# Optimization experiments

Measured on AMD Instinct MI355X. Metric: run time of the kernel, lower is better.

The kernel has to match this reference:

```python
import jax, jax.numpy as jnp
import numpy as np

HIDDEN = 2048
N_HEADS = 32
N_KV_HEADS = 8
HEAD_DIM = HIDDEN // N_HEADS  # 64
KV_GROUPS = N_HEADS // N_KV_HEADS  # 4
ROPE_THETA = 10000.0
BSZ, SEQ = 2, 2048


def setup_inputs() -> dict:
    key = jax.random.key(0)
    ks = jax.random.split(key, 5)
    s = 0.02
    hidden_states = jax.random.normal(ks[0], (BSZ, SEQ, HIDDEN), jnp.float32)
    position_ids = jnp.broadcast_to(jnp.arange(SEQ, dtype=jnp.int32), (BSZ, SEQ))
    Wq = jax.random.normal(ks[1], (HIDDEN, HIDDEN), jnp.float32) * s
    Wk = jax.random.normal(ks[2], (N_KV_HEADS * HEAD_DIM, HIDDEN), jnp.float32) * s
    Wv = jax.random.normal(ks[3], (N_KV_HEADS * HEAD_DIM, HIDDEN), jnp.float32) * s
    Wo = jax.random.normal(ks[4], (HIDDEN, HIDDEN), jnp.float32) * s
    return {"hidden_states": hidden_states, "position_ids": position_ids,
            "Wq": Wq, "Wk": Wk, "Wv": Wv, "Wo": Wo}


def _rope_cos_sin(position_ids):
    # Llama rotary embedding: inv_freq over even dims, emb = [freqs, freqs]
    inv_freq = 1.0 / (ROPE_THETA ** (jnp.arange(0, HEAD_DIM, 2, dtype=jnp.float32) / HEAD_DIM))  # [Hd/2]
    freqs = position_ids.astype(jnp.float32)[..., None] * inv_freq  # [B, S, Hd/2]
    emb = jnp.concatenate([freqs, freqs], axis=-1)  # [B, S, Hd]
    return jnp.cos(emb), jnp.sin(emb)


def _rotate_half(x):
    x1, x2 = jnp.split(x, 2, axis=-1)
    return jnp.concatenate([-x2, x1], axis=-1)


def reference(hidden_states, position_ids, Wq, Wk, Wv, Wo):
    bsz, seq_len, _ = hidden_states.shape
    # projections (nn.Linear: y = x @ W.T)
    q = (hidden_states @ Wq.T).reshape(bsz, seq_len, N_HEADS, HEAD_DIM).transpose(0, 2, 1, 3)
    k = (hidden_states @ Wk.T).reshape(bsz, seq_len, N_KV_HEADS, HEAD_DIM).transpose(0, 2, 1, 3)
    v = (hidden_states @ Wv.T).reshape(bsz, seq_len, N_KV_HEADS, HEAD_DIM).transpose(0, 2, 1, 3)
    cos, sin = _rope_cos_sin(position_ids)  # [B, S, Hd]
    cos = cos[:, None, :, :]
    sin = sin[:, None, :, :]
    q = q * cos + _rotate_half(q) * sin
    k = k * cos + _rotate_half(k) * sin
    # GQA expand kv heads to full head count
    k = jnp.repeat(k, KV_GROUPS, axis=1)  # [B, H, S, Hd]
    v = jnp.repeat(v, KV_GROUPS, axis=1)
    # naive full-softmax attention (no causal mask, matching the source)
    scores = jnp.einsum('bhqd,bhkd->bhqk', q, k) / jnp.sqrt(jnp.float32(HEAD_DIM))
    attn_w = jax.nn.softmax(scores, axis=-1)
    attn_o = jnp.einsum('bhqk,bhkd->bhqd', attn_w, v)
    attn_o = attn_o.transpose(0, 2, 1, 3).reshape(bsz, seq_len, HIDDEN)
    return attn_o @ Wo.T
```

## Files before the change

### kernel.cpp

```cpp
#include <hip/hip_runtime.h>
#include <hip/hip_bf16.h>
#include <stdint.h>

#define HID 2048
#define NH 32
#define NKV 8
#define HD 64
#define BSZ 2
#define SEQ 2048
#define NROWS (BSZ*SEQ)
#define KVCOLS (NKV*HD)
#define QKVN 3072

typedef __attribute__((ext_vector_type(8))) short bf16x8;
typedef __attribute__((ext_vector_type(4))) float f32x4;
typedef __attribute__((ext_vector_type(16))) float f32x16;
typedef __attribute__((ext_vector_type(2))) unsigned int u32x2;

__device__ __forceinline__ unsigned short f2bf(float f) {
  union { float f; uint32_t u; } v; v.f = f;
  uint32_t r = v.u + 0x7FFFu + ((v.u >> 16) & 1u);
  return (unsigned short)(r >> 16);
}

__device__ __forceinline__ unsigned pack_bf16(float a, float b) {
  union { __hip_bfloat162 h; unsigned u; } cv;
  cv.h = __float22bfloat162_rn(make_float2(a, b));
  return cv.u;
}

__device__ __forceinline__ float sum16(const f32x16& s) {
  float a0 = s[0] + s[1], a1 = s[2] + s[3], a2 = s[4] + s[5], a3 = s[6] + s[7];
  float a4 = s[8] + s[9], a5 = s[10] + s[11], a6 = s[12] + s[13], a7 = s[14] + s[15];
  float b0 = a0 + a1, b1 = a2 + a3, b2 = a4 + a5, b3 = a6 + a7;
  return (b0 + b1) + (b2 + b3);
}

#define MKPB(S, B0) ({ \
  unsigned A_ = pack_bf16((S)[B0], (S)[(B0)+1]); \
  unsigned C_ = pack_bf16((S)[(B0)+2], (S)[(B0)+3]); \
  unsigned B_ = pack_bf16((S)[(B0)+4], (S)[(B0)+5]); \
  unsigned D_ = pack_bf16((S)[(B0)+6], (S)[(B0)+7]); \
  u32x2 r0_ = __builtin_amdgcn_permlane32_swap(A_, B_, false, false); \
  u32x2 r1_ = __builtin_amdgcn_permlane32_swap(C_, D_, false, false); \
  union { uint4 u; bf16x8 v; } cv_; \
  cv_.u.x = r0_.x; cv_.u.y = r1_.x; cv_.u.z = r0_.y; cv_.u.w = r1_.y; \
  cv_.v; })

__global__ __launch_bounds__(256) void cvt_kernel(const float* __restrict__ in,
                                                  unsigned short* __restrict__ out, int n) {
  int idx = (blockIdx.x * 256 + threadIdx.x) * 4;
  int stride = gridDim.x * 256 * 4;
  for (int i = idx; i < n; i += stride) {
    float4 v = *(const float4*)(in + i);
    ushort4 o;
    o.x = f2bf(v.x); o.y = f2bf(v.y); o.z = f2bf(v.z); o.w = f2bf(v.w);
    *(ushort4*)(out + i) = o;
  }
}

#define BM 128
#define BN 128
#define BK 32

__global__ __launch_bounds__(256) void gemm_btn(
    const unsigned short* __restrict__ A,
    const unsigned short* __restrict__ B,
    float* __restrict__ C,
    int M, int N, int K)
{
  __shared__ unsigned short As[2][BM * BK];
  __shared__ unsigned short Bs[2][BN * BK];
  const int t = threadIdx.x;
  const int w = t >> 6, l = t & 63;
  const int wr = w >> 1, wc = w & 1;

  const int nwg = gridDim.x * gridDim.y;
  const int lin = blockIdx.y * gridDim.x + blockIdx.x;
  const int swz = (lin & 7) * (nwg >> 3) + (lin >> 3);
  const int bx = swz % gridDim.x, by = swz / gridDim.x;

  const int row0 = by * BM, col0 = bx * BN;
  const int lr = l & 15, lk = (l >> 4) * 8;

  f32x4 acc[4][4];
  for (int i = 0; i < 4; ++i)
    for (int j = 0; j < 4; ++j)
      acc[i][j] = (f32x4){0.f, 0.f, 0.f, 0.f};

  auto stage = [&](int bi, int k0) {
    #pragma unroll
    for (int i = 0; i < 2; ++i) {
      int ebase = i * 2048 + w * 512;
      int e = ebase + l * 8;
      const unsigned short* srcA = A + (size_t)(row0 + (e >> 5)) * K + k0 + (e & 31);
      const unsigned short* srcB = B + (size_t)(col0 + (e >> 5)) * K + k0 + (e & 31);
      __builtin_amdgcn_global_load_lds((const __attribute__((address_space(1))) void*)srcA,
          (__attribute__((address_space(3))) void*)&As[bi][ebase], 16, 0, 0);
      __builtin_amdgcn_global_load_lds((const __attribute__((address_space(1))) void*)srcB,
          (__attribute__((address_space(3))) void*)&Bs[bi][ebase], 16, 0, 0);
    }
  };

  stage(0, 0);
  __syncthreads();
  int bi = 0;
  for (int k0 = 0; k0 < K; k0 += BK) {
    if (k0 + BK < K) stage(bi ^ 1, k0 + BK);
    bf16x8 a[4], b[4];
    #pragma unroll
    for (int mi = 0; mi < 4; ++mi)
      a[mi] = *(const bf16x8*)&As[bi][(wr * 64 + mi * 16 + lr) * BK + lk];
    #pragma unroll
    for (int ni = 0; ni < 4; ++ni)
      b[ni] = *(const bf16x8*)&Bs[bi][(wc * 64 + ni * 16 + lr) * BK + lk];
    #pragma unroll
    for (int mi = 0; mi < 4; ++mi)
      #pragma unroll
      for (int ni = 0; ni < 4; ++ni)
        acc[mi][ni] = __builtin_amdgcn_mfma_f32_16x16x32_bf16(a[mi], b[ni], acc[mi][ni], 0, 0, 0);
    __syncthreads();
    bi ^= 1;
  }

  const int crow = (l >> 4) * 4, ccol = l & 15;
  #pragma unroll
  for (int mi = 0; mi < 4; ++mi)
    #pragma unroll
    for (int ni = 0; ni < 4; ++ni) {
      float* cp = C + (size_t)(row0 + wr * 64 + mi * 16 + crow) * N + col0 + wc * 64 + ni * 16 + ccol;
      #pragma unroll
      for (int r = 0; r < 4; ++r)
        cp[(size_t)r * N] = acc[mi][ni][r];
    }
}

__global__ __launch_bounds__(256) void rope_k_kernel(const float* __restrict__ QKVf,
                                                     const int* __restrict__ pos_ids,
                                                     unsigned short* __restrict__ Kb) {
  int row = blockIdx.x;
  int t = threadIdx.x;
  int kh = t >> 5, j = t & 31;
  int b = row >> 11, s = row & 2047;
  float pos = (float)pos_ids[row];
  float invf = exp2f((float)j * -0.41524101186092029f);
  float sn, c;
  __sincosf(pos * invf, &sn, &c);
  const float* kr = QKVf + (size_t)row * QKVN + HID + kh * 64;
  float k1 = kr[j], k2 = kr[j + 32];
  float o1 = k1 * c - k2 * sn;
  float o2 = k2 * c + k1 * sn;
  unsigned short* outp = Kb + ((size_t)(b * NKV + kh) * SEQ + s) * HD;
  outp[j] = f2bf(o1);
  outp[j + 32] = f2bf(o2);
}

__global__ __launch_bounds__(256) void vt_kernel(const float* __restrict__ QKVf,
                                                 unsigned short* __restrict__ Vt) {
  int bid = blockIdx.x;
  int stile = bid & 31;
  int kh = (bid >> 5) & 7;
  int b = bid >> 8;
  int s0 = stile * 64;
  __shared__ unsigned short Ts[64][65];
  int t = threadIdx.x;
  {
    int r = t >> 2;
    int dq = (t & 3) * 16;
    const float* src = QKVf + (size_t)(b * SEQ + s0 + r) * QKVN + (HID + KVCOLS) + kh * 64 + dq;
    #pragma unroll
    for (int i = 0; i < 4; ++i) {
      float4 v = *(const float4*)(src + i * 4);
      Ts[r][dq + i * 4 + 0] = f2bf(v.x);
      Ts[r][dq + i * 4 + 1] = f2bf(v.y);
      Ts[r][dq + i * 4 + 2] = f2bf(v.z);
      Ts[r][dq + i * 4 + 3] = f2bf(v.w);
    }
  }
  __syncthreads();
  {
    int d = t >> 2;
    int cb = (t & 3) * 16;
    unsigned short* dst = Vt + ((size_t)(b * NKV + kh) * 64 + d) * SEQ + s0 + cb;
    #pragma unroll
    for (int i = 0; i < 4; ++i) {
      ushort4 o;
      o.x = Ts[cb + i * 4 + 0][d];
      o.y = Ts[cb + i * 4 + 1][d];
      o.z = Ts[cb + i * 4 + 2][d];
      o.w = Ts[cb + i * 4 + 3][d];
      *(ushort4*)(dst + i * 4) = o;
    }
  }
}

__global__ __launch_bounds__(512, 4) void attn_kernel(
    const float* __restrict__ QKVf,
    const int* __restrict__ pos_ids,
    const unsigned short* __restrict__ Kb,
    const unsigned short* __restrict__ Vt,
    unsigned short* __restrict__ AO)
{
  __shared__ unsigned short Ks[2][64 * 64];
  __shared__ unsigned short Vs[2][64 * 64];

  const int lin = blockIdx.x;
  const int bid = (lin & 7) * 64 + (lin >> 3);
  const int qtile = bid & 7;
  const int h = (bid >> 3) & 31;
  const int b = bid >> 8;
  const int kh = h >> 2;
  const int t = threadIdx.x, w = t >> 6, l = t & 63;
  const int lq = l & 31, hi = l >> 5;
  const int sw = (lq & 7) << 4;
  const int qrow = qtile * 256 + w * 32 + lq;

  bf16x8 qf[4];
  {
    const float SCL = 0.18033688011112042f;
    const float* Qsrc = QKVf + (size_t)(b * SEQ + qrow) * QKVN + h * 64;
    float pos = (float)pos_ids[b * SEQ + qrow];
    #pragma unroll
    for (int dk = 0; dk < 2; ++dk) {
      float4 a0 = *(const float4*)(Qsrc + dk * 16 + hi * 8);
      float4 a1 = *(const float4*)(Qsrc + dk * 16 + hi * 8 + 4);
      float4 b0 = *(const float4*)(Qsrc + 32 + dk * 16 + hi * 8);
      float4 b1 = *(const float4*)(Qsrc + 32 + dk * 16 + hi * 8 + 4);
      float x1[8] = {a0.x, a0.y, a0.z, a0.w, a1.x, a1.y, a1.z, a1.w};
      float x2[8] = {b0.x, b0.y, b0.z, b0.w, b1.x, b1.y, b1.z, b1.w};
      union { bf16x8 v; unsigned short us[8]; } lov, hiv;
      #pragma unroll
      for (int jj = 0; jj < 8; ++jj) {
        float jidx = (float)(dk * 16 + hi * 8 + jj);
        float sn, cs;
        __sincosf(pos * exp2f(jidx * -0.41524101186092029f), &sn, &cs);
        lov.us[jj] = f2bf((x1[jj] * cs - x2[jj] * sn) * SCL);
        hiv.us[jj] = f2bf((x2[jj] * cs + x1[jj] * sn) * SCL);
      }
      qf[dk] = lov.v;
      qf[dk + 2] = hiv.v;
    }
  }

  const unsigned short* Kt  = Kb + (size_t)(b * NKV + kh) * SEQ * HD;
  const unsigned short* Vth = Vt + (size_t)(b * NKV + kh) * HD * SEQ;

  const int dest = t * 16;
  const int srow = dest >> 7;
  const int scol = dest & 127;
  const int wdest = dest ^ ((srow & 7) << 4);
  const char* KsrcBase = (const char*)Kt + dest;
  const char* VsrcBase = (const char*)(Vth + (size_t)srow * SEQ) + scol;

  uint4 kreg, vreg;
  auto issue = [&](int kv0) {
    kreg = *(const uint4*)(KsrcBase + (size_t)kv0 * 128);
    vreg = *(const uint4*)(VsrcBase + kv0 * 2);
  };
  auto lwrite = [&](int si) {
    *(uint4*)((char*)Ks[si] + wdest) = kreg;
    *(uint4*)((char*)Vs[si] + wdest) = vreg;
  };

  const f32x16 Z = {0,0,0,0,0,0,0,0,0,0,0,0,0,0,0,0};
  float lsum = 0.f;
  f32x16 o0 = Z, o1 = Z;

  issue(0);
  lwrite(0);
  __syncthreads();

  int bi = 0;
  for (int it = 0; it < SEQ / 64; ++it) {
    const bool more = (it + 1 < SEQ / 64);
    if (more) issue((it + 1) * 64);

    const char* Kp = (const char*)Ks[bi];
    const char* Vp = (const char*)Vs[bi];

    f32x16 s0, s1;
    __builtin_amdgcn_s_setprio(1);
    {
      bf16x8 kf0 = *(const bf16x8*)(Kp + lq * 128 + ((hi * 16) ^ sw));
      bf16x8 kf1 = *(const bf16x8*)(Kp + 4096 + lq * 128 + ((hi * 16) ^ sw));
      s0 = __builtin_amdgcn_mfma_f32_32x32x16_bf16(kf0, qf[0], Z, 0, 0, 0);
      s1 = __builtin_amdgcn_mfma_f32_32x32x16_bf16(kf1, qf[0], Z, 0, 0, 0);
    }
    #pragma unroll
    for (int dk = 1; dk < 4; ++dk) {
      const int cb = dk * 32 + hi * 16;
      bf16x8 kf0 = *(const bf16x8*)(Kp + lq * 128 + (cb ^ sw));
      bf16x8 kf1 = *(const bf16x8*)(Kp + 4096 + lq * 128 + (cb ^ sw));
      s0 = __builtin_amdgcn_mfma_f32_32x32x16_bf16(kf0, qf[dk], s0, 0, 0, 0);
      s1 = __builtin_amdgcn_mfma_f32_32x32x16_bf16(kf1, qf[dk], s1, 0, 0, 0);
    }
    __builtin_amdgcn_s_setprio(0);

    #pragma unroll
    for (int r = 0; r < 16; ++r) { s0[r] = exp2f(s0[r]); s1[r] = exp2f(s1[r]); }
    float rs = sum16(s0) + sum16(s1);
    rs += __shfl_xor(rs, 32);
    lsum += rs;

    bf16x8 pb0 = MKPB(s0, 0), pb1 = MKPB(s0, 8), pb2 = MKPB(s1, 0), pb3 = MKPB(s1, 8);

    __builtin_amdgcn_s_setprio(1);
    #pragma unroll
    for (int ks = 0; ks < 4; ++ks) {
      const int cb = ks * 32 + hi * 16;
      bf16x8 vf0 = *(const bf16x8*)(Vp + lq * 128 + (cb ^ sw));
      bf16x8 vf1 = *(const bf16x8*)(Vp + 4096 + lq * 128 + (cb ^ sw));
      bf16x8 pa = (ks == 0) ? pb0 : (ks == 1) ? pb1 : (ks == 2) ? pb2 : pb3;
      o0 = __builtin_amdgcn_mfma_f32_32x32x16_bf16(vf0, pa, o0, 0, 0, 0);
      o1 = __builtin_amdgcn_mfma_f32_32x32x16_bf16(vf1, pa, o1, 0, 0, 0);
    }
    __builtin_amdgcn_s_setprio(0);

    if (more) lwrite(bi ^ 1);
    __syncthreads();
    bi ^= 1;
  }

  const float inv = 1.0f / lsum;
  unsigned short* op = AO + ((size_t)(b * SEQ) + qrow) * HID + h * 64;
  #pragma unroll
  for (int r = 0; r < 16; r += 2) {
    const int d = (r & 3) + 8 * (r >> 2) + 4 * hi;
    *(unsigned*)(op + d)      = pack_bf16(o0[r] * inv, o0[r + 1] * inv);
    *(unsigned*)(op + 32 + d) = pack_bf16(o1[r] * inv, o1[r + 1] * inv);
  }
}

extern "C" void kernel_launch(void* const* d_in, const int* in_sizes, int n_in,
                              void* d_out, int out_size, void* d_ws, size_t ws_size,
                              hipStream_t stream) {
  const float* hs  = (const float*)d_in[0];
  const int*   pos = (const int*)d_in[1];
  const float* Wq  = (const float*)d_in[2];
  const float* Wk  = (const float*)d_in[3];
  const float* Wv  = (const float*)d_in[4];
  const float* Wo  = (const float*)d_in[5];
  float* out = (float*)d_out;

  char* ws = (char*)d_ws;
  size_t off = 0;
  auto carve = [&](size_t bytes) { void* p = ws + off; off += (bytes + 255) & ~(size_t)255; return p; };

  unsigned short* Xb    = (unsigned short*)carve((size_t)NROWS * HID * 2);
  unsigned short* Wqkvb = (unsigned short*)carve((size_t)QKVN * HID * 2);
  unsigned short* Wob   = (unsigned short*)carve((size_t)HID * HID * 2);
  float*          QKVf  = (float*)carve((size_t)NROWS * QKVN * 4);
  unsigned short* Kbh   = (unsigned short*)carve((size_t)NROWS * KVCOLS * 2);
  unsigned short* Vtb   = (unsigned short*)carve((size_t)NROWS * KVCOLS * 2);
  unsigned short* AO    = (unsigned short*)carve((size_t)NROWS * HID * 2);

  cvt_kernel<<<1024, 256, 0, stream>>>(hs, Xb, NROWS * HID);
  cvt_kernel<<<512, 256, 0, stream>>>(Wq, Wqkvb, HID * HID);
  cvt_kernel<<<256, 256, 0, stream>>>(Wk, Wqkvb + (size_t)HID * HID, KVCOLS * HID);
  cvt_kernel<<<256, 256, 0, stream>>>(Wv, Wqkvb + (size_t)(HID + KVCOLS) * HID, KVCOLS * HID);
  cvt_kernel<<<512, 256, 0, stream>>>(Wo, Wob, HID * HID);

  gemm_btn<<<dim3(QKVN / BN, NROWS / BM), 256, 0, stream>>>(Xb, Wqkvb, QKVf, NROWS, QKVN, HID);

  rope_k_kernel<<<NROWS, 256, 0, stream>>>(QKVf, pos, Kbh);
  vt_kernel<<<BSZ * NKV * (SEQ / 64), 256, 0, stream>>>(QKVf, Vtb);

  attn_kernel<<<BSZ * NH * (SEQ / 256), 512, 0, stream>>>(QKVf, pos, Kbh, Vtb, AO);

  gemm_btn<<<dim3(HID / BN, NROWS / BM), 256, 0, stream>>>(AO, Wob, out, NROWS, HID, HID);
}
```

Measured before the change: 256.1 us.

## Fuse RoPE, Q scaling and V transpose into the QKV GEMM epilogue

```diff
diff --git a/kernel.cpp b/kernel.cpp
--- a/kernel.cpp
+++ b/kernel.cpp
@@ -46,6 +46,9 @@
   union { uint4 u; bf16x8 v; } cv_; \
   cv_.u.x = r0_.x; cv_.u.y = r1_.x; cv_.u.z = r0_.y; cv_.u.w = r1_.y; \
   cv_.v; })
+
+#define ROPE_C (-0.41524101186092029f)
+#define QSCL 0.18033688011112042f
 
 __global__ __launch_bounds__(256) void cvt_kernel(const float* __restrict__ in,
                                                   unsigned short* __restrict__ out, int n) {
@@ -135,68 +138,122 @@
     }
 }
 
-__global__ __launch_bounds__(256) void rope_k_kernel(const float* __restrict__ QKVf,
-                                                     const int* __restrict__ pos_ids,
-                                                     unsigned short* __restrict__ Kb) {
-  int row = blockIdx.x;
-  int t = threadIdx.x;
-  int kh = t >> 5, j = t & 31;
-  int b = row >> 11, s = row & 2047;
-  float pos = (float)pos_ids[row];
-  float invf = exp2f((float)j * -0.41524101186092029f);
-  float sn, c;
-  __sincosf(pos * invf, &sn, &c);
-  const float* kr = QKVf + (size_t)row * QKVN + HID + kh * 64;
-  float k1 = kr[j], k2 = kr[j + 32];
-  float o1 = k1 * c - k2 * sn;
-  float o2 = k2 * c + k1 * sn;
-  unsigned short* outp = Kb + ((size_t)(b * NKV + kh) * SEQ + s) * HD;
-  outp[j] = f2bf(o1);
-  outp[j + 32] = f2bf(o2);
-}
-
-__global__ __launch_bounds__(256) void vt_kernel(const float* __restrict__ QKVf,
-                                                 unsigned short* __restrict__ Vt) {
-  int bid = blockIdx.x;
-  int stile = bid & 31;
-  int kh = (bid >> 5) & 7;
-  int b = bid >> 8;
-  int s0 = stile * 64;
-  __shared__ unsigned short Ts[64][65];
-  int t = threadIdx.x;
-  {
-    int r = t >> 2;
-    int dq = (t & 3) * 16;
-    const float* src = QKVf + (size_t)(b * SEQ + s0 + r) * QKVN + (HID + KVCOLS) + kh * 64 + dq;
-    #pragma unroll
-    for (int i = 0; i < 4; ++i) {
-      float4 v = *(const float4*)(src + i * 4);
-      Ts[r][dq + i * 4 + 0] = f2bf(v.x);
-      Ts[r][dq + i * 4 + 1] = f2bf(v.y);
-      Ts[r][dq + i * 4 + 2] = f2bf(v.z);
-      Ts[r][dq + i * 4 + 3] = f2bf(v.w);
-    }
-  }
+__global__ __launch_bounds__(256) void gemm_qkv(
+    const unsigned short* __restrict__ A,
+    const unsigned short* __restrict__ B,
+    const int* __restrict__ pos_ids,
+    unsigned short* __restrict__ Qb,
+    unsigned short* __restrict__ Kb,
+    unsigned short* __restrict__ Vt)
+{
+  __shared__ unsigned short As[2][BM * BK];
+  __shared__ unsigned short Bs[2][BN * BK];
+  const int t = threadIdx.x;
+  const int w = t >> 6, l = t & 63;
+  const int wr = w >> 1, wc = w & 1;
+
+  const int nwg = gridDim.x * gridDim.y;
+  const int lin = blockIdx.y * gridDim.x + blockIdx.x;
+  const int swz = (lin & 7) * (nwg >> 3) + (lin >> 3);
+  const int bx = swz % gridDim.x, by = swz / gridDim.x;
+
+  const int row0 = by * BM, col0 = bx * BN;
+  const int lr = l & 15, lk = (l >> 4) * 8;
+
+  f32x4 acc[4][4];
+  for (int i = 0; i < 4; ++i)
+    for (int j = 0; j < 4; ++j)
+      acc[i][j] = (f32x4){0.f, 0.f, 0.f, 0.f};
+
+  auto stage = [&](int bi, int k0) {
+    #pragma unroll
+    for (int i = 0; i < 2; ++i) {
+      int ebase = i * 2048 + w * 512;
+      int e = ebase + l * 8;
+      const unsigned short* srcA = A + (size_t)(row0 + (e >> 5)) * HID + k0 + (e & 31);
+      const unsigned short* srcB = B + (size_t)(col0 + (e >> 5)) * HID + k0 + (e & 31);
+      __builtin_amdgcn_global_load_lds((const __attribute__((address_space(1))) void*)srcA,
+          (__attribute__((address_space(3))) void*)&As[bi][ebase], 16, 0, 0);
+      __builtin_amdgcn_global_load_lds((const __attribute__((address_space(1))) void*)srcB,
+          (__attribute__((address_space(3))) void*)&Bs[bi][ebase], 16, 0, 0);
+    }
+  };
+
+  stage(0, 0);
   __syncthreads();
-  {
-    int d = t >> 2;
-    int cb = (t & 3) * 16;
-    unsigned short* dst = Vt + ((size_t)(b * NKV + kh) * 64 + d) * SEQ + s0 + cb;
-    #pragma unroll
-    for (int i = 0; i < 4; ++i) {
-      ushort4 o;
-      o.x = Ts[cb + i * 4 + 0][d];
-      o.y = Ts[cb + i * 4 + 1][d];
-      o.z = Ts[cb + i * 4 + 2][d];
-      o.w = Ts[cb + i * 4 + 3][d];
-      *(ushort4*)(dst + i * 4) = o;
+  int bi = 0;
+  for (int k0 = 0; k0 < HID; k0 += BK) {
+    if (k0 + BK < HID) stage(bi ^ 1, k0 + BK);
+    bf16x8 a[4], b[4];
+    #pragma unroll
+    for (int mi = 0; mi < 4; ++mi)
+      a[mi] = *(const bf16x8*)&As[bi][(wr * 64 + mi * 16 + lr) * BK + lk];
+    #pragma unroll
+    for (int ni = 0; ni < 4; ++ni)
+      b[ni] = *(const bf16x8*)&Bs[bi][(wc * 64 + ni * 16 + lr) * BK + lk];
+    #pragma unroll
+    for (int mi = 0; mi < 4; ++mi)
+      #pragma unroll
+      for (int ni = 0; ni < 4; ++ni)
+        acc[mi][ni] = __builtin_amdgcn_mfma_f32_16x16x32_bf16(a[mi], b[ni], acc[mi][ni], 0, 0, 0);
+    __syncthreads();
+    bi ^= 1;
+  }
+
+  const int crow = (l >> 4) * 4, ccol = l & 15;
+  const int colbase = col0 + wc * 64;
+  const int b = row0 >> 11;
+
+  if (colbase < HID + KVCOLS) {
+    const bool isQ = colbase < HID;
+    const float scl = isQ ? QSCL : 1.0f;
+    const int hh = (isQ ? colbase : colbase - HID) >> 6;
+    unsigned short* base = (isQ ? Qb + ((size_t)(b * NH + hh) * SEQ) * HD
+                                : Kb + ((size_t)(b * NKV + hh) * SEQ) * HD);
+    const float invf0 = exp2f((float)ccol * ROPE_C);
+    const float invf1 = exp2f((float)(ccol + 16) * ROPE_C);
+    #pragma unroll
+    for (int mi = 0; mi < 4; ++mi) {
+      const int rowb = row0 + wr * 64 + mi * 16 + crow;
+      #pragma unroll
+      for (int r = 0; r < 4; ++r) {
+        const int row = rowb + r;
+        const int s = row & (SEQ - 1);
+        const float pos = (float)pos_ids[row];
+        #pragma unroll
+        for (int ni = 0; ni < 2; ++ni) {
+          float sn, cs;
+          __sincosf(pos * (ni ? invf1 : invf0), &sn, &cs);
+          const float x1 = acc[mi][ni][r], x2 = acc[mi][ni + 2][r];
+          unsigned short* p = base + (size_t)s * HD + ni * 16 + ccol;
+          p[0]  = f2bf((x1 * cs - x2 * sn) * scl);
+          p[32] = f2bf((x2 * cs + x1 * sn) * scl);
+        }
+      }
+    }
+  } else {
+    const int cv = colbase - (HID + KVCOLS);
+    const int kh = cv >> 6;
+    unsigned short* vbase = Vt + ((size_t)(b * NKV + kh) * HD) * SEQ;
+    #pragma unroll
+    for (int mi = 0; mi < 4; ++mi) {
+      const int s = (row0 + wr * 64 + mi * 16 + crow) & (SEQ - 1);
+      #pragma unroll
+      for (int ni = 0; ni < 4; ++ni) {
+        const int d = (cv & 63) + ni * 16 + ccol - (cv & 63);
+        ushort4 o;
+        o.x = f2bf(acc[mi][ni][0]);
+        o.y = f2bf(acc[mi][ni][1]);
+        o.z = f2bf(acc[mi][ni][2]);
+        o.w = f2bf(acc[mi][ni][3]);
+        *(ushort4*)(vbase + (size_t)(ni * 16 + ccol) * SEQ + s) = o;
+      }
     }
   }
 }
 
 __global__ __launch_bounds__(512, 4) void attn_kernel(
-    const float* __restrict__ QKVf,
-    const int* __restrict__ pos_ids,
+    const unsigned short* __restrict__ Qb,
     const unsigned short* __restrict__ Kb,
     const unsigned short* __restrict__ Vt,
     unsigned short* __restrict__ AO)
@@ -217,29 +274,10 @@
 
   bf16x8 qf[4];
   {
-    const float SCL = 0.18033688011112042f;
-    const float* Qsrc = QKVf + (size_t)(b * SEQ + qrow) * QKVN + h * 64;
-    float pos = (float)pos_ids[b * SEQ + qrow];
-    #pragma unroll
-    for (int dk = 0; dk < 2; ++dk) {
-      float4 a0 = *(const float4*)(Qsrc + dk * 16 + hi * 8);
-      float4 a1 = *(const float4*)(Qsrc + dk * 16 + hi * 8 + 4);
-      float4 b0 = *(const float4*)(Qsrc + 32 + dk * 16 + hi * 8);
-      float4 b1 = *(const float4*)(Qsrc + 32 + dk * 16 + hi * 8 + 4);
-      float x1[8] = {a0.x, a0.y, a0.z, a0.w, a1.x, a1.y, a1.z, a1.w};
-      float x2[8] = {b0.x, b0.y, b0.z, b0.w, b1.x, b1.y, b1.z, b1.w};
-      union { bf16x8 v; unsigned short us[8]; } lov, hiv;
-      #pragma unroll
-      for (int jj = 0; jj < 8; ++jj) {
-        float jidx = (float)(dk * 16 + hi * 8 + jj);
-        float sn, cs;
-        __sincosf(pos * exp2f(jidx * -0.41524101186092029f), &sn, &cs);
-        lov.us[jj] = f2bf((x1[jj] * cs - x2[jj] * sn) * SCL);
-        hiv.us[jj] = f2bf((x2[jj] * cs + x1[jj] * sn) * SCL);
-      }
-      qf[dk] = lov.v;
-      qf[dk + 2] = hiv.v;
-    }
+    const unsigned short* Qrow = Qb + ((size_t)(b * NH + h) * SEQ + qrow) * HD;
+    #pragma unroll
+    for (int dk = 0; dk < 4; ++dk)
+      qf[dk] = *(const bf16x8*)(Qrow + dk * 16 + hi * 8);
   }
 
   const unsigned short* Kt  = Kb + (size_t)(b * NKV + kh) * SEQ * HD;
@@ -349,7 +387,7 @@
   unsigned short* Xb    = (unsigned short*)carve((size_t)NROWS * HID * 2);
   unsigned short* Wqkvb = (unsigned short*)carve((size_t)QKVN * HID * 2);
   unsigned short* Wob   = (unsigned short*)carve((size_t)HID * HID * 2);
-  float*          QKVf  = (float*)carve((size_t)NROWS * QKVN * 4);
+  unsigned short* Qbh   = (unsigned short*)carve((size_t)NROWS * HID * 2);
   unsigned short* Kbh   = (unsigned short*)carve((size_t)NROWS * KVCOLS * 2);
   unsigned short* Vtb   = (unsigned short*)carve((size_t)NROWS * KVCOLS * 2);
   unsigned short* AO    = (unsigned short*)carve((size_t)NROWS * HID * 2);
@@ -360,12 +398,9 @@
   cvt_kernel<<<256, 256, 0, stream>>>(Wv, Wqkvb + (size_t)(HID + KVCOLS) * HID, KVCOLS * HID);
   cvt_kernel<<<512, 256, 0, stream>>>(Wo, Wob, HID * HID);
 
-  gemm_btn<<<dim3(QKVN / BN, NROWS / BM), 256, 0, stream>>>(Xb, Wqkvb, QKVf, NROWS, QKVN, HID);
-
-  rope_k_kernel<<<NROWS, 256, 0, stream>>>(QKVf, pos, Kbh);
-  vt_kernel<<<BSZ * NKV * (SEQ / 64), 256, 0, stream>>>(QKVf, Vtb);
-
-  attn_kernel<<<BSZ * NH * (SEQ / 256), 512, 0, stream>>>(QKVf, pos, Kbh, Vtb, AO);
+  gemm_qkv<<<dim3(QKVN / BN, NROWS / BM), 256, 0, stream>>>(Xb, Wqkvb, pos, Qbh, Kbh, Vtb);
+
+  attn_kernel<<<BSZ * NH * (SEQ / 256), 512, 0, stream>>>(Qbh, Kbh, Vtb, AO);
 
   gemm_btn<<<dim3(HID / BN, NROWS / BM), 256, 0, stream>>>(AO, Wob, out, NROWS, HID, HID);
 }
```

New measurement: 272.1 us. 6.3% more time.
